# Kernel optimization log

Measured on AMD Instinct MI355X. Metric: run time of the kernel, lower is better.

The kernel has to match this reference:

```python
import jax, jax.numpy as jnp
import numpy as np

SIM_THRESHOLD = 0.9


def setup_inputs() -> dict:
    key = jax.random.key(0)
    k1, k2 = jax.random.split(key)
    # patches: b * c * num * ws * ws  (b=2, c=8, num=1024, ws=3) -> n = 16384
    patches = jax.random.normal(k1, (2, 8, 1024, 3, 3), dtype=jnp.float32)
    # db: m * ws * ws
    db = jax.random.normal(k2, (16384, 3, 3), dtype=jnp.float32)
    return {"patches": patches, "db": db}


def reference(patches, db):
    ws = patches.shape[-1]
    p = patches.reshape(-1, ws, ws)          # [n, ws, ws]
    n = p.shape[0]
    m = db.shape[0]
    pf = p.reshape(n, -1)                    # [n, ws*ws]
    df = db.reshape(m, -1)                   # [m, ws*ws]
    dot = pf @ df.T                          # [n, m], tiny K=ws*ws -> memory bound
    norm_n = jnp.linalg.norm(pf, axis=1, keepdims=True)   # [n, 1]
    norm_m = jnp.linalg.norm(df, axis=1, keepdims=True)   # [m, 1]
    cos = dot / (norm_n * norm_m.T)          # [n, m] cosine similarity
    # patch kept only if dissimilar to EVERY db entry
    mask = jnp.all(cos < SIM_THRESHOLD, axis=1)            # [n] bool
    # jit-friendly fixed-shape compaction: zero out rejected patches instead of
    # dropping rows (original does db = cat(db, patches[mask]))
    filtered = jnp.where(mask[:, None, None], p, jnp.zeros((), p.dtype))
    return jnp.concatenate([db.reshape(-1, ws, ws), filtered], axis=0)  # [m+n, ws, ws]
```

## Files before the change

kernel.cpp:

```cpp
#include <hip/hip_runtime.h>

#define NPATCH 16384
#define NDB    16384
#define WS9    9
#define KP     16
#define JCH    32
#define CHUNK  (NDB / JCH)
#define TILES  (CHUNK / 32)
#define BAND_LO 0.8998f
#define BAND_HI 0.9002f
#define COPY_BLOCKS 144

typedef short bf16x8 __attribute__((ext_vector_type(8)));
typedef float f32x16 __attribute__((ext_vector_type(16)));

__device__ __forceinline__ float np_norm9(const float* v) {
#pragma clang fp contract(off)
    float q0 = v[0] * v[0], q1 = v[1] * v[1], q2 = v[2] * v[2], q3 = v[3] * v[3];
    float q4 = v[4] * v[4], q5 = v[5] * v[5], q6 = v[6] * v[6], q7 = v[7] * v[7];
    float q8 = v[8] * v[8];
    float s = ((q0 + q1) + (q2 + q3)) + ((q4 + q5) + (q6 + q7));
    s = s + q8;
    return sqrtf(s);
}

__device__ __forceinline__ unsigned short f2bf(float x) {
    unsigned u = __float_as_uint(x);
    return (unsigned short)((u + 0x7fffu + ((u >> 16) & 1u)) >> 16);
}
__device__ __forceinline__ float bf2f(unsigned short h) {
    return __uint_as_float(((unsigned)h) << 16);
}

__device__ __forceinline__ void stage_row(const float* __restrict__ src,
                                          unsigned short* dh, unsigned short* dl) {
    float v[WS9];
#pragma unroll
    for (int k = 0; k < WS9; k++) v[k] = src[k];
    float inv = 1.0f / np_norm9(v);
    unsigned short h[KP], l[KP];
#pragma unroll
    for (int k = 0; k < KP; k++) {
        float x = (k < WS9) ? v[k] * inv : 0.0f;
        h[k] = f2bf(x);
        l[k] = f2bf(x - bf2f(h[k]));
    }
    int hw[8], lw[8];
#pragma unroll
    for (int k = 0; k < 8; k++) {
        hw[k] = (int)h[2 * k] | ((int)h[2 * k + 1] << 16);
        lw[k] = (int)l[2 * k] | ((int)l[2 * k + 1] << 16);
    }
    ((int4*)dh)[0] = make_int4(hw[0], hw[1], hw[2], hw[3]);
    ((int4*)dh)[1] = make_int4(hw[4], hw[5], hw[6], hw[7]);
    ((int4*)dl)[0] = make_int4(lw[0], lw[1], lw[2], lw[3]);
    ((int4*)dl)[1] = make_int4(lw[4], lw[5], lw[6], lw[7]);
}

__global__ __launch_bounds__(256) void k_phase1(const float* __restrict__ patches,
                                                const float* __restrict__ db,
                                                float* __restrict__ partial,
                                                int* __restrict__ band_count) {
    __shared__ __align__(16) unsigned short s_dnh[CHUNK * KP];
    __shared__ __align__(16) unsigned short s_dnl[CHUNK * KP];
    __shared__ __align__(16) unsigned short s_pnh[256 * KP];
    __shared__ __align__(16) unsigned short s_pnl[256 * KP];

    if (blockIdx.x == 0 && blockIdx.y == 0 && threadIdx.x == 0) *band_count = 0;

    int jbase = blockIdx.y * CHUNK;
    int ibase = blockIdx.x * 256;
#pragma unroll
    for (int rr = 0; rr < CHUNK / 256; rr++) {
        int r = rr * 256 + threadIdx.x;
        stage_row(db + (size_t)(jbase + r) * WS9, &s_dnh[r * KP], &s_dnl[r * KP]);
    }
    stage_row(patches + (size_t)(ibase + threadIdx.x) * WS9,
              &s_pnh[threadIdx.x * KP], &s_pnl[threadIdx.x * KP]);
    __syncthreads();

    int lane = threadIdx.x & 63;
    int wave = threadIdx.x >> 6;
    int col = lane & 31;
    int half = lane >> 5;
    int i0 = ibase + wave * 64;

    const bf16x8* Ph = (const bf16x8*)s_pnh;
    const bf16x8* Pl = (const bf16x8*)s_pnl;
    bf16x8 b_hi0 = Ph[(wave * 64 + col) * 2 + half];
    bf16x8 b_lo0 = Pl[(wave * 64 + col) * 2 + half];
    bf16x8 b_hi1 = Ph[(wave * 64 + 32 + col) * 2 + half];
    bf16x8 b_lo1 = Pl[(wave * 64 + 32 + col) * 2 + half];

    const bf16x8* Ah = (const bf16x8*)s_dnh;
    const bf16x8* Al = (const bf16x8*)s_dnl;

    f32x16 zc = {0.f,0.f,0.f,0.f,0.f,0.f,0.f,0.f,0.f,0.f,0.f,0.f,0.f,0.f,0.f,0.f};
    float rm0 = -3.0e38f, rm1 = -3.0e38f;

#pragma unroll 2
    for (int t = 0; t < TILES; ++t) {
        bf16x8 a_h = Ah[(t * 32 + col) * 2 + half];
        bf16x8 a_l = Al[(t * 32 + col) * 2 + half];
        f32x16 acc0 = __builtin_amdgcn_mfma_f32_32x32x16_bf16(a_h, b_hi0, zc, 0, 0, 0);
        acc0 = __builtin_amdgcn_mfma_f32_32x32x16_bf16(a_h, b_lo0, acc0, 0, 0, 0);
        acc0 = __builtin_amdgcn_mfma_f32_32x32x16_bf16(a_l, b_hi0, acc0, 0, 0, 0);
        f32x16 acc1 = __builtin_amdgcn_mfma_f32_32x32x16_bf16(a_h, b_hi1, zc, 0, 0, 0);
        acc1 = __builtin_amdgcn_mfma_f32_32x32x16_bf16(a_h, b_lo1, acc1, 0, 0, 0);
        acc1 = __builtin_amdgcn_mfma_f32_32x32x16_bf16(a_l, b_hi1, acc1, 0, 0, 0);
#pragma unroll
        for (int r = 0; r < 16; ++r) {
            rm0 = fmaxf(rm0, acc0[r]);
            rm1 = fmaxf(rm1, acc1[r]);
        }
    }
    rm0 = fmaxf(rm0, __shfl_xor(rm0, 32, 64));
    rm1 = fmaxf(rm1, __shfl_xor(rm1, 32, 64));
    int ti = half ? (i0 + 32 + col) : (i0 + col);
    partial[(size_t)blockIdx.y * NPATCH + ti] = half ? rm1 : rm0;
}

__global__ __launch_bounds__(256) void k_finish(const float* __restrict__ patches,
                                                const float* __restrict__ db,
                                                const float* __restrict__ partial,
                                                float* __restrict__ out,
                                                int* __restrict__ band_list,
                                                int* __restrict__ band_count) {
    int b = blockIdx.x;
    if (b < COPY_BLOCKS) {
        int e = b * 256 + threadIdx.x;
        ((float4*)out)[e] = ((const float4*)db)[e];
        return;
    }
    int i = (b - COPY_BLOCKS) * 256 + threadIdx.x;
    float cosmax = partial[i];
#pragma unroll
    for (int c = 1; c < JCH; c++) cosmax = fmaxf(cosmax, partial[(size_t)c * NPATCH + i]);
    if (cosmax >= BAND_LO && cosmax < BAND_HI) {
        int idx = atomicAdd(band_count, 1);
        band_list[idx] = i;
        return;
    }
    int hit = (cosmax >= BAND_HI) ? 1 : 0;
#pragma unroll
    for (int k = 0; k < WS9; k++)
        out[(size_t)(NDB + i) * WS9 + k] = hit ? 0.0f : patches[i * WS9 + k];
}

__global__ __launch_bounds__(256) void k_phase2(const float* __restrict__ patches,
                                                const float* __restrict__ db,
                                                const int* __restrict__ band_list,
                                                const int* __restrict__ band_count,
                                                float* __restrict__ out) {
    __shared__ float sp[WS9];
    __shared__ float snp;
    __shared__ int shit;
    int nb = *band_count;
    for (int idx = blockIdx.x; idx < nb; idx += gridDim.x) {
        int i = band_list[idx];
        if (threadIdx.x == 0) {
            float p[WS9];
            for (int k = 0; k < WS9; k++) { p[k] = patches[i * WS9 + k]; sp[k] = p[k]; }
            snp = np_norm9(p);
            shit = 0;
        }
        __syncthreads();
        float p[WS9];
#pragma unroll
        for (int k = 0; k < WS9; k++) p[k] = sp[k];
        float npn = snp;
        int hit = 0;
        for (int j = (int)threadIdx.x; j < NDB; j += 256) {
            float d[WS9];
#pragma unroll
            for (int k = 0; k < WS9; k++) d[k] = db[j * WS9 + k];
            float dot = 0.0f;
#pragma unroll
            for (int k = 0; k < WS9; k++) dot = fmaf(p[k], d[k], dot);
            float nd = np_norm9(d);
            float cs = dot / (npn * nd);
            if (!((double)cs < 0.9)) hit = 1;
        }
        if (hit) atomicOr(&shit, 1);
        __syncthreads();
        int m = shit;
        if (threadIdx.x < WS9)
            out[(size_t)(NDB + i) * WS9 + threadIdx.x] = m ? 0.0f : sp[threadIdx.x];
        __syncthreads();
    }
}

extern "C" void kernel_launch(void* const* d_in, const int* in_sizes, int n_in,
                              void* d_out, int out_size, void* d_ws, size_t ws_size,
                              hipStream_t stream) {
    const float* patches = (const float*)d_in[0];
    const float* db      = (const float*)d_in[1];
    float* out = (float*)d_out;

    char* wsb = (char*)d_ws;
    float* partial    = (float*)wsb;
    int*   band_list  = (int*)(wsb + (size_t)JCH * NPATCH * 4);
    int*   band_count = (int*)(wsb + (size_t)JCH * NPATCH * 4 + (size_t)NPATCH * 4);

    k_phase1<<<dim3(NPATCH / 256, JCH), dim3(256), 0, stream>>>(patches, db,
                                                                partial, band_count);
    k_finish<<<dim3(COPY_BLOCKS + NPATCH / 256), dim3(256), 0, stream>>>(
        patches, db, partial, out, band_list, band_count);
    k_phase2<<<dim3(256), dim3(256), 0, stream>>>(patches, db, band_list, band_count, out);
}
```

Before: 98.32 us.

## Fuse band re-check into finish kernel with per-block shared band list

Removes the third kernel launch by handling borderline (near-threshold) patches inside k_finish, using a block-local shared-memory list instead of a global atomic counter and list. The db copy is spread across the 64 finish blocks rather than run by dedicated copy blocks, and the band_count reset in phase1 goes away. This saves a launch and the global atomics, but each block now rechecks its own band patches serially over all 16384 db rows. That path can be slow if one block gets many band patches, and the grid shrinks to 64 blocks.

```diff
diff --git a/kernel.cpp b/kernel.cpp
--- a/kernel.cpp
+++ b/kernel.cpp
@@ -9,7 +9,6 @@
 #define TILES  (CHUNK / 32)
 #define BAND_LO 0.8998f
 #define BAND_HI 0.9002f
-#define COPY_BLOCKS 144
 
 typedef short bf16x8 __attribute__((ext_vector_type(8)));
 typedef float f32x16 __attribute__((ext_vector_type(16)));
@@ -59,14 +58,11 @@
 
 __global__ __launch_bounds__(256) void k_phase1(const float* __restrict__ patches,
                                                 const float* __restrict__ db,
-                                                float* __restrict__ partial,
-                                                int* __restrict__ band_count) {
+                                                float* __restrict__ partial) {
     __shared__ __align__(16) unsigned short s_dnh[CHUNK * KP];
     __shared__ __align__(16) unsigned short s_dnl[CHUNK * KP];
     __shared__ __align__(16) unsigned short s_pnh[256 * KP];
     __shared__ __align__(16) unsigned short s_pnl[256 * KP];
-
-    if (blockIdx.x == 0 && blockIdx.y == 0 && threadIdx.x == 0) *band_count = 0;
 
     int jbase = blockIdx.y * CHUNK;
     int ibase = blockIdx.x * 256;
@@ -123,57 +119,54 @@
 __global__ __launch_bounds__(256) void k_finish(const float* __restrict__ patches,
                                                 const float* __restrict__ db,
                                                 const float* __restrict__ partial,
-                                                float* __restrict__ out,
-                                                int* __restrict__ band_list,
-                                                int* __restrict__ band_count) {
-    int b = blockIdx.x;
-    if (b < COPY_BLOCKS) {
-        int e = b * 256 + threadIdx.x;
-        ((float4*)out)[e] = ((const float4*)db)[e];
-        return;
+                                                float* __restrict__ out) {
+    __shared__ int s_list[256];
+    __shared__ int s_cnt;
+    __shared__ int s_hit;
+    if (threadIdx.x == 0) s_cnt = 0;
+    __syncthreads();
+
+    {
+        const float4* dbv = (const float4*)db;
+        float4* outv = (float4*)out;
+        int base = blockIdx.x * 576;
+#pragma unroll
+        for (int rr = 0; rr < 3; rr++) {
+            int t = rr * 256 + (int)threadIdx.x;
+            if (t < 576) outv[base + t] = dbv[base + t];
+        }
     }
-    int i = (b - COPY_BLOCKS) * 256 + threadIdx.x;
+
+    int i = blockIdx.x * 256 + threadIdx.x;
     float cosmax = partial[i];
 #pragma unroll
-    for (int c = 1; c < JCH; c++) cosmax = fmaxf(cosmax, partial[(size_t)c * NPATCH + i]);
+    for (int c = 1; c < JCH; c++)
+        cosmax = fmaxf(cosmax, partial[(size_t)c * NPATCH + i]);
     if (cosmax >= BAND_LO && cosmax < BAND_HI) {
-        int idx = atomicAdd(band_count, 1);
-        band_list[idx] = i;
-        return;
+        int idx = atomicAdd(&s_cnt, 1);
+        s_list[idx] = i;
+    } else {
+        int hit = (cosmax >= BAND_HI) ? 1 : 0;
+#pragma unroll
+        for (int k = 0; k < WS9; k++)
+            out[(size_t)(NDB + i) * WS9 + k] = hit ? 0.0f : patches[(size_t)i * WS9 + k];
     }
-    int hit = (cosmax >= BAND_HI) ? 1 : 0;
-#pragma unroll
-    for (int k = 0; k < WS9; k++)
-        out[(size_t)(NDB + i) * WS9 + k] = hit ? 0.0f : patches[i * WS9 + k];
-}
+    __syncthreads();
 
-__global__ __launch_bounds__(256) void k_phase2(const float* __restrict__ patches,
-                                                const float* __restrict__ db,
-                                                const int* __restrict__ band_list,
-                                                const int* __restrict__ band_count,
-                                                float* __restrict__ out) {
-    __shared__ float sp[WS9];
-    __shared__ float snp;
-    __shared__ int shit;
-    int nb = *band_count;
-    for (int idx = blockIdx.x; idx < nb; idx += gridDim.x) {
-        int i = band_list[idx];
-        if (threadIdx.x == 0) {
-            float p[WS9];
-            for (int k = 0; k < WS9; k++) { p[k] = patches[i * WS9 + k]; sp[k] = p[k]; }
-            snp = np_norm9(p);
-            shit = 0;
-        }
+    int nb = s_cnt;
+    for (int e = 0; e < nb; e++) {
+        int ip = s_list[e];
+        if (threadIdx.x == 0) s_hit = 0;
         __syncthreads();
         float p[WS9];
 #pragma unroll
-        for (int k = 0; k < WS9; k++) p[k] = sp[k];
-        float npn = snp;
+        for (int k = 0; k < WS9; k++) p[k] = patches[(size_t)ip * WS9 + k];
+        float npn = np_norm9(p);
         int hit = 0;
         for (int j = (int)threadIdx.x; j < NDB; j += 256) {
             float d[WS9];
 #pragma unroll
-            for (int k = 0; k < WS9; k++) d[k] = db[j * WS9 + k];
+            for (int k = 0; k < WS9; k++) d[k] = db[(size_t)j * WS9 + k];
             float dot = 0.0f;
 #pragma unroll
             for (int k = 0; k < WS9; k++) dot = fmaf(p[k], d[k], dot);
@@ -181,11 +174,11 @@
             float cs = dot / (npn * nd);
             if (!((double)cs < 0.9)) hit = 1;
         }
-        if (hit) atomicOr(&shit, 1);
+        if (hit) atomicOr(&s_hit, 1);
         __syncthreads();
-        int m = shit;
+        int m = s_hit;
         if (threadIdx.x < WS9)
-            out[(size_t)(NDB + i) * WS9 + threadIdx.x] = m ? 0.0f : sp[threadIdx.x];
+            out[(size_t)(NDB + ip) * WS9 + threadIdx.x] = m ? 0.0f : p[threadIdx.x];
         __syncthreads();
     }
 }
@@ -197,14 +190,8 @@
     const float* db      = (const float*)d_in[1];
     float* out = (float*)d_out;
 
-    char* wsb = (char*)d_ws;
-    float* partial    = (float*)wsb;
-    int*   band_list  = (int*)(wsb + (size_t)JCH * NPATCH * 4);
-    int*   band_count = (int*)(wsb + (size_t)JCH * NPATCH * 4 + (size_t)NPATCH * 4);
+    float* partial = (float*)d_ws;
 
-    k_phase1<<<dim3(NPATCH / 256, JCH), dim3(256), 0, stream>>>(patches, db,
-                                                                partial, band_count);
-    k_finish<<<dim3(COPY_BLOCKS + NPATCH / 256), dim3(256), 0, stream>>>(
-        patches, db, partial, out, band_list, band_count);
-    k_phase2<<<dim3(256), dim3(256), 0, stream>>>(patches, db, band_list, band_count, out);
+    k_phase1<<<dim3(NPATCH / 256, JCH), dim3(256), 0, stream>>>(patches, db, partial);
+    k_finish<<<dim3(64), dim3(256), 0, stream>>>(patches, db, partial, out);
 }
```

Result: slower. 116.3 us (+18.3%).
